# Performance work log

Hardware: AMD Instinct MI355X
Metric: run time of the kernel (lower is better)

## Reference

```python
import jax, jax.numpy as jnp
import numpy as np

HEADS = 8
DIM_HEAD = 64
INNER = HEADS * DIM_HEAD  # 512
DIM = 256
MSA_H = 128  # number of MSA rows
MSA_W = 256  # sequence length


def setup_inputs() -> dict:
    key = jax.random.key(0)
    ks = jax.random.split(key, 8)
    n = MSA_H * MSA_W
    w_std = 0.02
    return {
        "x": jax.random.normal(ks[0], (1, n, DIM), dtype=jnp.float32),
        "wq_w": jax.random.normal(ks[1], (DIM, INNER), dtype=jnp.float32) * w_std,
        "wkv_w": jax.random.normal(ks[2], (DIM, 2 * INNER), dtype=jnp.float32) * w_std,
        "wout_w": jax.random.normal(ks[3], (INNER, DIM), dtype=jnp.float32) * w_std,
        "wout_b": jnp.zeros((DIM,), dtype=jnp.float32),
        "hq_w": jax.random.normal(ks[4], (DIM, INNER), dtype=jnp.float32) * w_std,
        "hkv_w": jax.random.normal(ks[5], (DIM, 2 * INNER), dtype=jnp.float32) * w_std,
        "hout_w": jax.random.normal(ks[6], (INNER, DIM), dtype=jnp.float32) * w_std,
        "hout_b": jnp.zeros((DIM,), dtype=jnp.float32),
        "msa_h": MSA_H,
        "msa_w": MSA_W,
    }


def reference(x, wq_w, wkv_w, wout_w, wout_b, hq_w, hkv_w, hout_w, hout_b, msa_h, msa_w):
    b, n, d = x.shape
    h, w = msa_h, msa_w
    scale = DIM_HEAD ** -0.5
    x4 = x.reshape(b, h, w, d)  # (b, rows, cols, dim)

    # ---- width attention: attend across MSA rows (h), independent per column (w) ----
    xw = jnp.swapaxes(x4, 1, 2)  # (b, w, h, d)
    q = (xw @ wq_w).reshape(b, w, h, HEADS, DIM_HEAD)
    kv = (xw @ wkv_w).reshape(b, w, h, 2, HEADS, DIM_HEAD)
    k, v = kv[..., 0, :, :], kv[..., 1, :, :]
    dots = jnp.einsum('bwiHd,bwjHd->bwHij', q, k) * scale  # (b, w, H, h, h)
    attn = jax.nn.softmax(dots, axis=-1)
    o = jnp.einsum('bwHij,bwjHd->bwiHd', attn, v).reshape(b, w, h, INNER)
    w_out = o @ wout_w + wout_b  # (b, w, h, d)
    w_out = jnp.swapaxes(w_out, 1, 2)  # (b, h, w, d)

    # ---- height attention: attend across columns (w), rows tied (tie_attn_dim = h) ----
    q = (x4 @ hq_w).reshape(b, h, w, HEADS, DIM_HEAD)
    kv = (x4 @ hkv_w).reshape(b, h, w, 2, HEADS, DIM_HEAD)
    k, v = kv[..., 0, :, :], kv[..., 1, :, :]
    tie_scale = scale * (h ** -0.5)
    # scores summed over tied row dim r: 'b r h i d, b r h j d -> b h i j'
    dots = jnp.einsum('briHd,brjHd->bHij', q, k) * tie_scale  # (b, H, w, w)
    attn = jax.nn.softmax(dots, axis=-1)
    o = jnp.einsum('bHij,brjHd->briHd', attn, v).reshape(b, h, w, INNER)
    h_out = o @ hout_w + hout_b  # (b, h, w, d)

    out = w_out + h_out
    return out.reshape(b, h * w, d)
```

## Files before the change

### kernel.cpp

```cpp
#include <hip/hip_runtime.h>

typedef short s16x8 __attribute__((ext_vector_type(8)));
typedef float f32x4 __attribute__((ext_vector_type(4)));

#define MFMA16(a, b, c) __builtin_amdgcn_mfma_f32_16x16x32_bf16((a), (b), (c), 0, 0, 0)

__device__ __forceinline__ unsigned short f2b(float f) {
  union { float f; unsigned int u; } v; v.f = f;
  unsigned int u = v.u;
  unsigned int r = (u + 0x7fffu + ((u >> 16) & 1u)) >> 16;
  return (unsigned short)r;
}
__device__ __forceinline__ float b2f(unsigned short b) {
  union { unsigned int u; float f; } v; v.u = ((unsigned int)b) << 16;
  return v.f;
}

__device__ __forceinline__ void gld_lds16(const void* g, void* l) {
  __builtin_amdgcn_global_load_lds(
      (const __attribute__((address_space(1))) unsigned int*)g,
      (__attribute__((address_space(3))) unsigned int*)l, 16, 0, 0);
}

__global__ __launch_bounds__(256) void cvt_x(const float* __restrict__ x,
                                             unsigned short* __restrict__ xb) {
  size_t i = ((size_t)blockIdx.x * 256 + threadIdx.x) * 4;
  float4 v = *(const float4*)(x + i);
  ushort4 o;
  o.x = f2b(v.x); o.y = f2b(v.y); o.z = f2b(v.z); o.w = f2b(v.w);
  *(ushort4*)(xb + i) = o;
}

__global__ __launch_bounds__(256) void build_wt(const float* __restrict__ wq,
                                                const float* __restrict__ wkv,
                                                const float* __restrict__ hq,
                                                const float* __restrict__ hkv,
                                                unsigned short* __restrict__ WT) {
  const int n = blockIdx.x, k = threadIdx.x;
  float v;
  if (n < 512)       v = wq [(size_t)k * 512  + n];
  else if (n < 1536) v = wkv[(size_t)k * 1024 + (n - 512)];
  else if (n < 2048) v = hq [(size_t)k * 512  + (n - 1536)];
  else               v = hkv[(size_t)k * 1024 + (n - 2048)];
  WT[(size_t)n * 256 + k] = f2b(v);
}

__global__ __launch_bounds__(256) void build_w2t(const float* __restrict__ wout,
                                                 const float* __restrict__ hout,
                                                 unsigned short* __restrict__ W2T) {
  const int n = blockIdx.x;
  for (int k = threadIdx.x; k < 1024; k += 256) {
    const float v = (k < 512) ? wout[(size_t)k * 256 + n] : hout[(size_t)(k - 512) * 256 + n];
    W2T[(size_t)n * 1024 + k] = f2b(v);
  }
}

__global__ __launch_bounds__(256) void gemm_qkv(const unsigned short* __restrict__ X,
                                                const unsigned short* __restrict__ WT,
                                                unsigned short* __restrict__ C,
                                                int branch) {
  __shared__ unsigned short As[128 * 32];
  __shared__ unsigned short Bs[128 * 32];
  const int tid = threadIdx.x, wave = tid >> 6, lane = tid & 63;
  const int q = lane >> 4, l = lane & 15;
  const int m0 = blockIdx.x * 128;
  const int n0 = blockIdx.y * 128;
  const int mt = (wave >> 1) * 64;
  const int nt = (wave & 1) * 64;
  const char* Xb = (const char*)X;
  const char* Wb = (const char*)WT;
  const int srow = wave * 32 + (lane >> 2);
  const int sboff = (lane & 3) * 16;
  char* AsB = (char*)As;
  char* BsB = (char*)Bs;
  f32x4 acc[4][4] = {};
#pragma unroll
  for (int ks = 0; ks < 8; ++ks) {
    const int kb = ks * 64;
    gld_lds16(Xb + (size_t)(m0 + srow) * 512 + kb + sboff, AsB + wave * 2048);
    gld_lds16(Xb + (size_t)(m0 + srow + 16) * 512 + kb + sboff, AsB + wave * 2048 + 1024);
    gld_lds16(Wb + (size_t)(n0 + srow) * 512 + kb + sboff, BsB + wave * 2048);
    gld_lds16(Wb + (size_t)(n0 + srow + 16) * 512 + kb + sboff, BsB + wave * 2048 + 1024);
    __syncthreads();
    s16x8 a[4], b[4];
#pragma unroll
    for (int i = 0; i < 4; ++i) a[i] = *(const s16x8*)(&As[(mt + i * 16 + l) * 32 + q * 8]);
#pragma unroll
    for (int j = 0; j < 4; ++j) b[j] = *(const s16x8*)(&Bs[(nt + j * 16 + l) * 32 + q * 8]);
#pragma unroll
    for (int i = 0; i < 4; ++i)
#pragma unroll
      for (int j = 0; j < 4; ++j) acc[i][j] = MFMA16(a[i], b[j], acc[i][j]);
    __syncthreads();
  }
#pragma unroll
  for (int i = 0; i < 4; ++i)
#pragma unroll
    for (int j = 0; j < 4; ++j) {
      const int col = n0 + nt + j * 16 + l;
      const int part = col >> 9, H = (col & 511) >> 6, d = col & 63;
      unsigned short* base = C + (size_t)part * 16777216;
#pragma unroll
      for (int r = 0; r < 4; ++r) {
        const int m = m0 + mt + i * 16 + q * 4 + r;
        size_t idx;
        if (branch == 0) idx = ((size_t)((m & 255) * 8 + H) * 128 + (m >> 8)) * 64 + d;
        else             idx = ((size_t)((m >> 8) * 8 + H) * 256 + (m & 255)) * 64 + d;
        base[idx] = f2b(acc[i][j][r]);
      }
    }
}

__global__ __launch_bounds__(256) void transpose_v(const unsigned short* __restrict__ V,
                                                   unsigned short* __restrict__ VT,
                                                   int J, int bpsShift) {
  __shared__ unsigned short T[128 * 72];
  const int tid = threadIdx.x;
  const int slab = blockIdx.x >> bpsShift;
  const int j0 = (blockIdx.x & ((1 << bpsShift) - 1)) * 128;
  const unsigned short* Vs = V + (size_t)slab * J * 64;
  unsigned short* VTs = VT + (size_t)slab * J * 64;
#pragma unroll
  for (int u = tid; u < 1024; u += 256) {
    const int j = u >> 3, db = u & 7;
    s16x8 v = *(const s16x8*)(Vs + (size_t)(j0 + j) * 64 + db * 8);
    *(s16x8*)(&T[j * 72 + db * 8]) = v;
  }
  __syncthreads();
#pragma unroll
  for (int it = 0; it < 4; ++it) {
    const int v = it * 256 + tid;
    const int d = v & 63, jb = v >> 6;
    unsigned short tmp[8];
#pragma unroll
    for (int t = 0; t < 8; ++t) tmp[t] = T[(jb * 8 + t) * 72 + d];
    *(s16x8*)(VTs + (size_t)d * J + j0 + jb * 8) = *(s16x8*)tmp;
  }
}

__global__ __launch_bounds__(256) void col_attn(const unsigned short* __restrict__ C,
                                                const unsigned short* __restrict__ VT,
                                                unsigned short* __restrict__ Ow) {
  __shared__ unsigned short Sp[128 * 136];
  const int w = blockIdx.x, H = blockIdx.y;
  const int tid = threadIdx.x, wave = tid >> 6, lane = tid & 63;
  const int q = lane >> 4, l = lane & 15;
  const size_t slab = (size_t)(w * 8 + H) * 8192;
  const unsigned short* Qs = C + slab;
  const unsigned short* Ks = C + 16777216 + slab;
  const unsigned short* VTs = VT + slab;
  const int m0 = wave * 32;
  f32x4 acc[2][8] = {};
#pragma unroll
  for (int ks = 0; ks < 2; ++ks) {
    const int kk = ks * 32 + q * 8;
    s16x8 a[2], b[8];
#pragma unroll
    for (int i = 0; i < 2; ++i) a[i] = *(const s16x8*)(Qs + (m0 + i * 16 + l) * 64 + kk);
#pragma unroll
    for (int j = 0; j < 8; ++j) b[j] = *(const s16x8*)(Ks + (j * 16 + l) * 64 + kk);
#pragma unroll
    for (int i = 0; i < 2; ++i)
#pragma unroll
      for (int j = 0; j < 8; ++j) acc[i][j] = MFMA16(a[i], b[j], acc[i][j]);
  }
#pragma unroll
  for (int i = 0; i < 2; ++i)
#pragma unroll
    for (int r = 0; r < 4; ++r) {
      float vj[8];
      float mx = -1e30f;
#pragma unroll
      for (int j = 0; j < 8; ++j) { vj[j] = acc[i][j][r] * 0.125f; mx = fmaxf(mx, vj[j]); }
      mx = fmaxf(mx, __shfl_xor(mx, 1, 64));
      mx = fmaxf(mx, __shfl_xor(mx, 2, 64));
      mx = fmaxf(mx, __shfl_xor(mx, 4, 64));
      mx = fmaxf(mx, __shfl_xor(mx, 8, 64));
      float s = 0.f;
#pragma unroll
      for (int j = 0; j < 8; ++j) { vj[j] = __expf(vj[j] - mx); s += vj[j]; }
      s += __shfl_xor(s, 1, 64);
      s += __shfl_xor(s, 2, 64);
      s += __shfl_xor(s, 4, 64);
      s += __shfl_xor(s, 8, 64);
      const float inv = 1.0f / s;
      const int row = m0 + i * 16 + q * 4 + r;
#pragma unroll
      for (int j = 0; j < 8; ++j) Sp[row * 136 + j * 16 + l] = f2b(vj[j] * inv);
    }
  __syncthreads();
  f32x4 o[2][4] = {};
#pragma unroll
  for (int ks = 0; ks < 4; ++ks) {
    const int kk = ks * 32 + q * 8;
    s16x8 a[2], b[4];
#pragma unroll
    for (int i = 0; i < 2; ++i) a[i] = *(const s16x8*)(&Sp[(m0 + i * 16 + l) * 136 + kk]);
#pragma unroll
    for (int j = 0; j < 4; ++j) b[j] = *(const s16x8*)(VTs + (j * 16 + l) * 128 + kk);
#pragma unroll
    for (int i = 0; i < 2; ++i)
#pragma unroll
      for (int j = 0; j < 4; ++j) o[i][j] = MFMA16(a[i], b[j], o[i][j]);
  }
#pragma unroll
  for (int i = 0; i < 2; ++i)
#pragma unroll
    for (int j = 0; j < 4; ++j)
#pragma unroll
      for (int r = 0; r < 4; ++r) {
        const int row = m0 + i * 16 + q * 4 + r;
        const int d = j * 16 + l;
        Ow[(size_t)(row * 256 + w) * 512 + H * 64 + d] = f2b(o[i][j][r]);
      }
}

__global__ __launch_bounds__(256) void row_dots(const unsigned short* __restrict__ C,
                                                float* __restrict__ dp) {
  const int H = blockIdx.z;
  const int r0 = blockIdx.y * 16;
  const int ti = blockIdx.x & 1, tj = blockIdx.x >> 1;
  const int tid = threadIdx.x, wave = tid >> 6, lane = tid & 63;
  const int q = lane >> 4, l = lane & 15;
  const int m0 = ti * 128 + (wave >> 1) * 64;
  const int n0 = tj * 128 + (wave & 1) * 64;
  const unsigned short* Qh = C;
  const unsigned short* Kh = C + 16777216;
  f32x4 acc[4][4] = {};
  for (int ks = 0; ks < 32; ++ks) {
    const int k = ks * 32 + q * 8;
    const int rr = r0 + (k >> 6), d = k & 63;
    const size_t slab = (size_t)(rr * 8 + H) * 16384;
    s16x8 a[4], b[4];
#pragma unroll
    for (int i = 0; i < 4; ++i) a[i] = *(const s16x8*)(Qh + slab + (m0 + i * 16 + l) * 64 + d);
#pragma unroll
    for (int j = 0; j < 4; ++j) b[j] = *(const s16x8*)(Kh + slab + (n0 + j * 16 + l) * 64 + d);
#pragma unroll
    for (int i = 0; i < 4; ++i)
#pragma unroll
      for (int j = 0; j < 4; ++j) acc[i][j] = MFMA16(a[i], b[j], acc[i][j]);
  }
  float* outp = dp + ((size_t)blockIdx.y * 8 + H) * 65536;
#pragma unroll
  for (int i = 0; i < 4; ++i)
#pragma unroll
    for (int j = 0; j < 4; ++j)
#pragma unroll
      for (int r = 0; r < 4; ++r)
        outp[(size_t)(m0 + i * 16 + q * 4 + r) * 256 + n0 + j * 16 + l] = acc[i][j][r];
}

__global__ __launch_bounds__(256) void row_softmax(const float* __restrict__ dp,
                                                   unsigned short* __restrict__ attn) {
  const int row = blockIdx.x;
  const int H = row >> 8, i = row & 255;
  const int t = threadIdx.x, wave = t >> 6, lane = t & 63;
  __shared__ float red[8];
  float v = 0.f;
#pragma unroll
  for (int c = 0; c < 8; ++c) v += dp[((size_t)c * 8 + H) * 65536 + (size_t)i * 256 + t];
  v *= 1.1048543456e-2f;
  float m = v;
  for (int o = 32; o > 0; o >>= 1) m = fmaxf(m, __shfl_xor(m, o, 64));
  if (lane == 0) red[wave] = m;
  __syncthreads();
  const float M = fmaxf(fmaxf(red[0], red[1]), fmaxf(red[2], red[3]));
  const float e = __expf(v - M);
  float s = e;
  for (int o = 32; o > 0; o >>= 1) s += __shfl_xor(s, o, 64);
  if (lane == 0) red[4 + wave] = s;
  __syncthreads();
  const float S = red[4] + red[5] + red[6] + red[7];
  attn[(size_t)row * 256 + t] = f2b(e / S);
}

__global__ __launch_bounds__(256) void row_pv(const unsigned short* __restrict__ attn,
                                              const unsigned short* __restrict__ VT,
                                              unsigned short* __restrict__ Oh) {
  const int r = blockIdx.x, H = blockIdx.y;
  const int tid = threadIdx.x, wave = tid >> 6, lane = tid & 63;
  const int q = lane >> 4, l = lane & 15;
  const unsigned short* VTs = VT + (size_t)(r * 8 + H) * 16384;
  const unsigned short* A = attn + (size_t)H * 65536;
  const int m0 = wave * 64;
  f32x4 acc[4][4] = {};
#pragma unroll
  for (int ks = 0; ks < 8; ++ks) {
    const int kk = ks * 32 + q * 8;
    s16x8 a[4], b[4];
#pragma unroll
    for (int i = 0; i < 4; ++i) a[i] = *(const s16x8*)(A + (size_t)(m0 + i * 16 + l) * 256 + kk);
#pragma unroll
    for (int j = 0; j < 4; ++j) b[j] = *(const s16x8*)(VTs + (j * 16 + l) * 256 + kk);
#pragma unroll
    for (int i = 0; i < 4; ++i)
#pragma unroll
      for (int j = 0; j < 4; ++j) acc[i][j] = MFMA16(a[i], b[j], acc[i][j]);
  }
#pragma unroll
  for (int i = 0; i < 4; ++i)
#pragma unroll
    for (int j = 0; j < 4; ++j)
#pragma unroll
      for (int rr = 0; rr < 4; ++rr) {
        const int iw = m0 + i * 16 + q * 4 + rr;
        const int d = j * 16 + l;
        Oh[(size_t)(r * 256 + iw) * 512 + H * 64 + d] = f2b(acc[i][j][rr]);
      }
}

__global__ __launch_bounds__(256) void out_proj(const unsigned short* __restrict__ Ow,
                                                const unsigned short* __restrict__ Oh,
                                                const unsigned short* __restrict__ W2T,
                                                const float* __restrict__ bw,
                                                const float* __restrict__ bh,
                                                float* __restrict__ out) {
  __shared__ unsigned short As[128 * 32];
  __shared__ unsigned short Bs[128 * 32];
  const int tid = threadIdx.x, wave = tid >> 6, lane = tid & 63;
  const int q = lane >> 4, l = lane & 15;
  const int m0 = blockIdx.x * 128;
  const int n0 = blockIdx.y * 128;
  const int mt = (wave >> 1) * 64;
  const int nt = (wave & 1) * 64;
  const char* OwB = (const char*)Ow;
  const char* OhB = (const char*)Oh;
  const char* Wb = (const char*)W2T;
  const int srow = wave * 32 + (lane >> 2);
  const int sboff = (lane & 3) * 16;
  char* AsB = (char*)As;
  char* BsB = (char*)Bs;
  f32x4 acc[4][4] = {};
  for (int ks = 0; ks < 32; ++ks) {
    const char* Ob = (ks < 16) ? OwB : OhB;
    const int kb = (ks & 15) * 64;
    gld_lds16(Ob + (size_t)(m0 + srow) * 1024 + kb + sboff, AsB + wave * 2048);
    gld_lds16(Ob + (size_t)(m0 + srow + 16) * 1024 + kb + sboff, AsB + wave * 2048 + 1024);
    gld_lds16(Wb + (size_t)(n0 + srow) * 2048 + ks * 64 + sboff, BsB + wave * 2048);
    gld_lds16(Wb + (size_t)(n0 + srow + 16) * 2048 + ks * 64 + sboff, BsB + wave * 2048 + 1024);
    __syncthreads();
    s16x8 a[4], b[4];
#pragma unroll
    for (int i = 0; i < 4; ++i) a[i] = *(const s16x8*)(&As[(mt + i * 16 + l) * 32 + q * 8]);
#pragma unroll
    for (int j = 0; j < 4; ++j) b[j] = *(const s16x8*)(&Bs[(nt + j * 16 + l) * 32 + q * 8]);
#pragma unroll
    for (int i = 0; i < 4; ++i)
#pragma unroll
      for (int j = 0; j < 4; ++j) acc[i][j] = MFMA16(a[i], b[j], acc[i][j]);
    __syncthreads();
  }
#pragma unroll
  for (int i = 0; i < 4; ++i)
#pragma unroll
    for (int j = 0; j < 4; ++j) {
      const int col = n0 + nt + j * 16 + l;
      const float bias = bw[col] + bh[col];
#pragma unroll
      for (int r = 0; r < 4; ++r)
        out[(size_t)(m0 + mt + i * 16 + q * 4 + r) * 256 + col] = acc[i][j][r] + bias;
    }
}

extern "C" void kernel_launch(void* const* d_in, const int* in_sizes, int n_in,
                              void* d_out, int out_size, void* d_ws, size_t ws_size,
                              hipStream_t stream) {
  const float* x    = (const float*)d_in[0];
  const float* wq   = (const float*)d_in[1];
  const float* wkv  = (const float*)d_in[2];
  const float* wout = (const float*)d_in[3];
  const float* bw   = (const float*)d_in[4];
  const float* hq   = (const float*)d_in[5];
  const float* hkv  = (const float*)d_in[6];
  const float* hout = (const float*)d_in[7];
  const float* bh   = (const float*)d_in[8];
  float* out = (float*)d_out;

  char* ws = (char*)d_ws;
  unsigned short* x_bf  = (unsigned short*)(ws);
  float*          dp    = (float*)(ws + 16777216);
  unsigned short* VT1   = (unsigned short*)(ws);
  unsigned short* WcatT = (unsigned short*)(ws + 33554432);
  unsigned short* W2T   = (unsigned short*)(ws + 35127296);
  unsigned short* attn  = (unsigned short*)(ws + 35651584);
  unsigned short* Ow    = (unsigned short*)(ws + 36700160);
  unsigned short* Oh    = (unsigned short*)(ws + 70254592);
  unsigned short* VT0   = Oh;
  unsigned short* Cproj = (unsigned short*)(ws + 103809024);

  cvt_x<<<8192, 256, 0, stream>>>(x, x_bf);
  build_wt<<<3072, 256, 0, stream>>>(wq, wkv, hq, hkv, WcatT);
  build_w2t<<<256, 256, 0, stream>>>(wout, hout, W2T);

  gemm_qkv<<<dim3(256, 12), 256, 0, stream>>>(x_bf, WcatT, Cproj, 0);
  transpose_v<<<2048, 256, 0, stream>>>(Cproj + (size_t)2 * 16777216, VT0, 128, 0);
  col_attn<<<dim3(256, 8), 256, 0, stream>>>(Cproj, VT0, Ow);
  gemm_qkv<<<dim3(256, 12), 256, 0, stream>>>(x_bf, WcatT + 1536 * 256, Cproj, 1);
  row_dots<<<dim3(4, 8, 8), 256, 0, stream>>>(Cproj, dp);
  row_softmax<<<2048, 256, 0, stream>>>(dp, attn);
  transpose_v<<<2048, 256, 0, stream>>>(Cproj + (size_t)2 * 16777216, VT1, 256, 1);
  row_pv<<<dim3(128, 8), 256, 0, stream>>>(attn, VT1, Oh);
  out_proj<<<dim3(256, 2), 256, 0, stream>>>(Ow, Oh, W2T, bw, bh, out);
}
```

Measured before the change: 397.5 us.

## Split col_attn and row_dots into single-wave blocks and fix LDS read layout

col_attn now runs as one-wave blocks, each handling a 32-row band of one column and head, which gives 8192 small blocks instead of 2048 four-wave ones. row_dots splits the tied-row reduction into 32 chunks of 4 rows, computed by single-wave 64x64 tiles, and writes partial sums into two scratch buffers that row_softmax then adds up. The GEMM staging changes the lane-to-row mapping for global_load_lds and reads fragments contiguously, to avoid LDS bank conflicts. The cost is more partial-sum traffic (4x the dp data, read back in softmax) and reuse of workspace regions for dp0 and dp1, which depends on buffer lifetimes not overlapping.

```diff
diff --git a/kernel.cpp b/kernel.cpp
--- a/kernel.cpp
+++ b/kernel.cpp
@@ -69,24 +69,24 @@
   const int nt = (wave & 1) * 64;
   const char* Xb = (const char*)X;
   const char* Wb = (const char*)WT;
-  const int srow = wave * 32 + (lane >> 2);
-  const int sboff = (lane & 3) * 16;
+  const int prow = lane & 15;
+  const int pchk = lane >> 4;
   char* AsB = (char*)As;
   char* BsB = (char*)Bs;
   f32x4 acc[4][4] = {};
 #pragma unroll
   for (int ks = 0; ks < 8; ++ks) {
     const int kb = ks * 64;
-    gld_lds16(Xb + (size_t)(m0 + srow) * 512 + kb + sboff, AsB + wave * 2048);
-    gld_lds16(Xb + (size_t)(m0 + srow + 16) * 512 + kb + sboff, AsB + wave * 2048 + 1024);
-    gld_lds16(Wb + (size_t)(n0 + srow) * 512 + kb + sboff, BsB + wave * 2048);
-    gld_lds16(Wb + (size_t)(n0 + srow + 16) * 512 + kb + sboff, BsB + wave * 2048 + 1024);
+    gld_lds16(Xb + (size_t)(m0 + wave * 32 + prow) * 512 + kb + pchk * 16, AsB + wave * 2048);
+    gld_lds16(Xb + (size_t)(m0 + wave * 32 + 16 + prow) * 512 + kb + pchk * 16, AsB + wave * 2048 + 1024);
+    gld_lds16(Wb + (size_t)(n0 + wave * 32 + prow) * 512 + kb + pchk * 16, BsB + wave * 2048);
+    gld_lds16(Wb + (size_t)(n0 + wave * 32 + 16 + prow) * 512 + kb + pchk * 16, BsB + wave * 2048 + 1024);
     __syncthreads();
     s16x8 a[4], b[4];
 #pragma unroll
-    for (int i = 0; i < 4; ++i) a[i] = *(const s16x8*)(&As[(mt + i * 16 + l) * 32 + q * 8]);
-#pragma unroll
-    for (int j = 0; j < 4; ++j) b[j] = *(const s16x8*)(&Bs[(nt + j * 16 + l) * 32 + q * 8]);
+    for (int i = 0; i < 4; ++i) a[i] = *(const s16x8*)(&As[(mt + i * 16) * 32 + (q * 16 + l) * 8]);
+#pragma unroll
+    for (int j = 0; j < 4; ++j) b[j] = *(const s16x8*)(&Bs[(nt + j * 16) * 32 + (q * 16 + l) * 8]);
 #pragma unroll
     for (int i = 0; i < 4; ++i)
 #pragma unroll
@@ -138,25 +138,24 @@
   }
 }
 
-__global__ __launch_bounds__(256) void col_attn(const unsigned short* __restrict__ C,
-                                                const unsigned short* __restrict__ VT,
-                                                unsigned short* __restrict__ Ow) {
-  __shared__ unsigned short Sp[128 * 136];
-  const int w = blockIdx.x, H = blockIdx.y;
-  const int tid = threadIdx.x, wave = tid >> 6, lane = tid & 63;
-  const int q = lane >> 4, l = lane & 15;
+__global__ __launch_bounds__(64) void col_attn(const unsigned short* __restrict__ C,
+                                               const unsigned short* __restrict__ VT,
+                                               unsigned short* __restrict__ Ow) {
+  __shared__ unsigned short Sp[32 * 136];
+  const int bx = blockIdx.x;
+  const int band = bx & 3, H = (bx >> 2) & 7, w = bx >> 5;
+  const int lane = threadIdx.x, q = lane >> 4, l = lane & 15;
   const size_t slab = (size_t)(w * 8 + H) * 8192;
-  const unsigned short* Qs = C + slab;
+  const unsigned short* Qs = C + slab + (size_t)band * 2048;
   const unsigned short* Ks = C + 16777216 + slab;
   const unsigned short* VTs = VT + slab;
-  const int m0 = wave * 32;
   f32x4 acc[2][8] = {};
 #pragma unroll
   for (int ks = 0; ks < 2; ++ks) {
     const int kk = ks * 32 + q * 8;
     s16x8 a[2], b[8];
 #pragma unroll
-    for (int i = 0; i < 2; ++i) a[i] = *(const s16x8*)(Qs + (m0 + i * 16 + l) * 64 + kk);
+    for (int i = 0; i < 2; ++i) a[i] = *(const s16x8*)(Qs + (i * 16 + l) * 64 + kk);
 #pragma unroll
     for (int j = 0; j < 8; ++j) b[j] = *(const s16x8*)(Ks + (j * 16 + l) * 64 + kk);
 #pragma unroll
@@ -184,7 +183,7 @@
       s += __shfl_xor(s, 4, 64);
       s += __shfl_xor(s, 8, 64);
       const float inv = 1.0f / s;
-      const int row = m0 + i * 16 + q * 4 + r;
+      const int row = i * 16 + q * 4 + r;
 #pragma unroll
       for (int j = 0; j < 8; ++j) Sp[row * 136 + j * 16 + l] = f2b(vj[j] * inv);
     }
@@ -195,7 +194,7 @@
     const int kk = ks * 32 + q * 8;
     s16x8 a[2], b[4];
 #pragma unroll
-    for (int i = 0; i < 2; ++i) a[i] = *(const s16x8*)(&Sp[(m0 + i * 16 + l) * 136 + kk]);
+    for (int i = 0; i < 2; ++i) a[i] = *(const s16x8*)(&Sp[(i * 16 + l) * 136 + kk]);
 #pragma unroll
     for (int j = 0; j < 4; ++j) b[j] = *(const s16x8*)(VTs + (j * 16 + l) * 128 + kk);
 #pragma unroll
@@ -209,25 +208,24 @@
     for (int j = 0; j < 4; ++j)
 #pragma unroll
       for (int r = 0; r < 4; ++r) {
-        const int row = m0 + i * 16 + q * 4 + r;
+        const int row = band * 32 + i * 16 + q * 4 + r;
         const int d = j * 16 + l;
         Ow[(size_t)(row * 256 + w) * 512 + H * 64 + d] = f2b(o[i][j][r]);
       }
 }
 
-__global__ __launch_bounds__(256) void row_dots(const unsigned short* __restrict__ C,
-                                                float* __restrict__ dp) {
-  const int H = blockIdx.z;
-  const int r0 = blockIdx.y * 16;
-  const int ti = blockIdx.x & 1, tj = blockIdx.x >> 1;
-  const int tid = threadIdx.x, wave = tid >> 6, lane = tid & 63;
-  const int q = lane >> 4, l = lane & 15;
-  const int m0 = ti * 128 + (wave >> 1) * 64;
-  const int n0 = tj * 128 + (wave & 1) * 64;
+__global__ __launch_bounds__(64) void row_dots(const unsigned short* __restrict__ C,
+                                               float* __restrict__ dp0,
+                                               float* __restrict__ dp1) {
+  const int bx = blockIdx.x;
+  const int tile = bx & 15, H = (bx >> 4) & 7, chunk = bx >> 7;
+  const int lane = threadIdx.x, q = lane >> 4, l = lane & 15;
+  const int m0 = (tile & 3) * 64, n0 = (tile >> 2) * 64;
+  const int r0 = chunk * 4;
   const unsigned short* Qh = C;
   const unsigned short* Kh = C + 16777216;
   f32x4 acc[4][4] = {};
-  for (int ks = 0; ks < 32; ++ks) {
+  for (int ks = 0; ks < 8; ++ks) {
     const int k = ks * 32 + q * 8;
     const int rr = r0 + (k >> 6), d = k & 63;
     const size_t slab = (size_t)(rr * 8 + H) * 16384;
@@ -241,7 +239,7 @@
 #pragma unroll
       for (int j = 0; j < 4; ++j) acc[i][j] = MFMA16(a[i], b[j], acc[i][j]);
   }
-  float* outp = dp + ((size_t)blockIdx.y * 8 + H) * 65536;
+  float* outp = ((chunk < 16) ? dp0 : dp1) + ((size_t)((chunk & 15) * 8 + H)) * 65536;
 #pragma unroll
   for (int i = 0; i < 4; ++i)
 #pragma unroll
@@ -251,7 +249,8 @@
         outp[(size_t)(m0 + i * 16 + q * 4 + r) * 256 + n0 + j * 16 + l] = acc[i][j][r];
 }
 
-__global__ __launch_bounds__(256) void row_softmax(const float* __restrict__ dp,
+__global__ __launch_bounds__(256) void row_softmax(const float* __restrict__ dp0,
+                                                   const float* __restrict__ dp1,
                                                    unsigned short* __restrict__ attn) {
   const int row = blockIdx.x;
   const int H = row >> 8, i = row & 255;
@@ -259,7 +258,9 @@
   __shared__ float red[8];
   float v = 0.f;
 #pragma unroll
-  for (int c = 0; c < 8; ++c) v += dp[((size_t)c * 8 + H) * 65536 + (size_t)i * 256 + t];
+  for (int c = 0; c < 16; ++c) v += dp0[((size_t)c * 8 + H) * 65536 + (size_t)i * 256 + t];
+#pragma unroll
+  for (int c = 0; c < 16; ++c) v += dp1[((size_t)c * 8 + H) * 65536 + (size_t)i * 256 + t];
   v *= 1.1048543456e-2f;
   float m = v;
   for (int o = 32; o > 0; o >>= 1) m = fmaxf(m, __shfl_xor(m, o, 64));
@@ -327,24 +328,24 @@
   const char* OwB = (const char*)Ow;
   const char* OhB = (const char*)Oh;
   const char* Wb = (const char*)W2T;
-  const int srow = wave * 32 + (lane >> 2);
-  const int sboff = (lane & 3) * 16;
+  const int prow = lane & 15;
+  const int pchk = lane >> 4;
   char* AsB = (char*)As;
   char* BsB = (char*)Bs;
   f32x4 acc[4][4] = {};
   for (int ks = 0; ks < 32; ++ks) {
     const char* Ob = (ks < 16) ? OwB : OhB;
     const int kb = (ks & 15) * 64;
-    gld_lds16(Ob + (size_t)(m0 + srow) * 1024 + kb + sboff, AsB + wave * 2048);
-    gld_lds16(Ob + (size_t)(m0 + srow + 16) * 1024 + kb + sboff, AsB + wave * 2048 + 1024);
-    gld_lds16(Wb + (size_t)(n0 + srow) * 2048 + ks * 64 + sboff, BsB + wave * 2048);
-    gld_lds16(Wb + (size_t)(n0 + srow + 16) * 2048 + ks * 64 + sboff, BsB + wave * 2048 + 1024);
+    gld_lds16(Ob + (size_t)(m0 + wave * 32 + prow) * 1024 + kb + pchk * 16, AsB + wave * 2048);
+    gld_lds16(Ob + (size_t)(m0 + wave * 32 + 16 + prow) * 1024 + kb + pchk * 16, AsB + wave * 2048 + 1024);
+    gld_lds16(Wb + (size_t)(n0 + wave * 32 + prow) * 2048 + ks * 64 + pchk * 16, BsB + wave * 2048);
+    gld_lds16(Wb + (size_t)(n0 + wave * 32 + 16 + prow) * 2048 + ks * 64 + pchk * 16, BsB + wave * 2048 + 1024);
     __syncthreads();
     s16x8 a[4], b[4];
 #pragma unroll
-    for (int i = 0; i < 4; ++i) a[i] = *(const s16x8*)(&As[(mt + i * 16 + l) * 32 + q * 8]);
-#pragma unroll
-    for (int j = 0; j < 4; ++j) b[j] = *(const s16x8*)(&Bs[(nt + j * 16 + l) * 32 + q * 8]);
+    for (int i = 0; i < 4; ++i) a[i] = *(const s16x8*)(&As[(mt + i * 16) * 32 + (q * 16 + l) * 8]);
+#pragma unroll
+    for (int j = 0; j < 4; ++j) b[j] = *(const s16x8*)(&Bs[(nt + j * 16) * 32 + (q * 16 + l) * 8]);
 #pragma unroll
     for (int i = 0; i < 4; ++i)
 #pragma unroll
@@ -379,7 +380,7 @@
 
   char* ws = (char*)d_ws;
   unsigned short* x_bf  = (unsigned short*)(ws);
-  float*          dp    = (float*)(ws + 16777216);
+  float*          dp0   = (float*)(ws);
   unsigned short* VT1   = (unsigned short*)(ws);
   unsigned short* WcatT = (unsigned short*)(ws + 33554432);
   unsigned short* W2T   = (unsigned short*)(ws + 35127296);
@@ -387,6 +388,7 @@
   unsigned short* Ow    = (unsigned short*)(ws + 36700160);
   unsigned short* Oh    = (unsigned short*)(ws + 70254592);
   unsigned short* VT0   = Oh;
+  float*          dp1   = (float*)(ws + 70254592);
   unsigned short* Cproj = (unsigned short*)(ws + 103809024);
 
   cvt_x<<<8192, 256, 0, stream>>>(x, x_bf);
@@ -395,10 +397,10 @@
 
   gemm_qkv<<<dim3(256, 12), 256, 0, stream>>>(x_bf, WcatT, Cproj, 0);
   transpose_v<<<2048, 256, 0, stream>>>(Cproj + (size_t)2 * 16777216, VT0, 128, 0);
-  col_attn<<<dim3(256, 8), 256, 0, stream>>>(Cproj, VT0, Ow);
+  col_attn<<<8192, 64, 0, stream>>>(Cproj, VT0, Ow);
   gemm_qkv<<<dim3(256, 12), 256, 0, stream>>>(x_bf, WcatT + 1536 * 256, Cproj, 1);
-  row_dots<<<dim3(4, 8, 8), 256, 0, stream>>>(Cproj, dp);
-  row_softmax<<<2048, 256, 0, stream>>>(dp, attn);
+  row_dots<<<4096, 64, 0, stream>>>(Cproj, dp0, dp1);
+  row_softmax<<<2048, 256, 0, stream>>>(dp0, dp1, attn);
   transpose_v<<<2048, 256, 0, stream>>>(Cproj + (size_t)2 * 16777216, VT1, 256, 1);
   row_pv<<<dim3(128, 8), 256, 0, stream>>>(attn, VT1, Oh);
   out_proj<<<dim3(256, 2), 256, 0, stream>>>(Ow, Oh, W2T, bw, bh, out);
```

Result: slower. 471.1 us (+18.5%).
